# Optimization experiments

Measured on AMD Instinct MI355X. Metric: run time of the kernel, lower is better.

The kernel has to match this reference:

```python
import jax, jax.numpy as jnp
import numpy as np

B, NF, D = 8192, 64, 128


def setup_inputs() -> dict:
    key = jax.random.key(0)
    k1, k2, k3, k4 = jax.random.split(key, 4)
    F = jax.random.normal(k1, (B, NF, D), dtype=jnp.float32)
    # interaction weight tensor (num_fields, num_fields, embedding_dim)
    W = jax.random.normal(k2, (NF, NF, D), dtype=jnp.float32) * 0.05
    # torch Linear weights (out_features, in_features); y = x @ W.T
    K_w = jax.random.normal(k3, (D, D), dtype=jnp.float32) * (1.0 / np.sqrt(D))
    Q_w = jax.random.normal(k4, (D, D), dtype=jnp.float32) * (1.0 / np.sqrt(D))
    return {"F": F, "W": W, "K_w": K_w, "Q_w": Q_w}


def reference(F, W, K_w, Q_w):
    # K(F): torch Linear without bias -> F @ K_w.T, shape [B, NF, D]
    Kf = jnp.einsum('bjd,ed->bje', F, K_w)
    # S = bmm(F, K(F)^T) -> [B, NF, NF]
    S = jnp.einsum('bid,bjd->bij', F, Kf)
    # (S.unsqueeze(-1) * W).sum(dim=2) without materializing [B,NF,NF,D]
    out = jnp.einsum('bij,ijd->bid', S, W)
    # residual: Q(F)
    out = out + jnp.einsum('bid,ed->bie', F, Q_w)
    return out
```

## Files before the change

kernel.cpp:

```cpp
#include <hip/hip_runtime.h>
#include <stdint.h>

typedef _Float16 f16x8 __attribute__((ext_vector_type(8)));
typedef _Float16 f16x4 __attribute__((ext_vector_type(4)));
typedef float    f32x4 __attribute__((ext_vector_type(4)));

#define NFIELD 64
#define DIM    128
#define BTOT   8192

__global__ void prep_kernel(const float* __restrict__ W,
                            const float* __restrict__ Kw,
                            const float* __restrict__ Qw,
                            _Float16* __restrict__ Wt,
                            _Float16* __restrict__ Kh,
                            _Float16* __restrict__ Qh) {
  const int blk = blockIdx.x, t = threadIdx.x;
  if (blk < NFIELD) {
    const float* Wi = W + (size_t)blk * NFIELD * DIM;
    _Float16* Wo = Wt + (size_t)blk * DIM * NFIELD;
    for (int idx = t; idx < DIM * NFIELD; idx += 256) {
      int d = idx >> 6, j = idx & 63;
      Wo[idx] = (_Float16)Wi[j * DIM + d];
    }
  } else if (blk == NFIELD) {
    for (int idx = t; idx < DIM * DIM; idx += 256) Kh[idx] = (_Float16)Kw[idx];
  } else {
    for (int idx = t; idx < DIM * DIM; idx += 256) Qh[idx] = (_Float16)Qw[idx];
  }
}

__global__ __launch_bounds__(256, 3)
void s_kernel(const float* __restrict__ F,
              const _Float16* __restrict__ Kh,
              _Float16* __restrict__ Sg, int c0) {
  __shared__ _Float16 sF[64 * 136];
  __shared__ float    sKf[64 * 132];
  const int t = threadIdx.x;
  const int lane = t & 63, wave = t >> 6;
  const int l15 = lane & 15, quad = lane >> 4;
  const int b = c0 + blockIdx.x;
  const float* Fb = F + (size_t)b * (NFIELD * DIM);

  for (int idx = t; idx < 2048; idx += 256) {
    float4 v = ((const float4*)Fb)[idx];
    int row = idx >> 5, c4 = idx & 31;
    f16x4 h;
    h[0] = (_Float16)v.x; h[1] = (_Float16)v.y; h[2] = (_Float16)v.z; h[3] = (_Float16)v.w;
    *(f16x4*)&sF[row * 136 + c4 * 4] = h;
  }
  __syncthreads();

  f16x8 afK[4];
#pragma unroll
  for (int kt = 0; kt < 4; ++kt)
    afK[kt] = *(const f16x8*)&sF[(wave * 16 + l15) * 136 + kt * 32 + quad * 8];
#pragma unroll
  for (int et = 0; et < 8; ++et) {
    const _Float16* kp = Kh + (et * 16 + l15) * DIM + quad * 8;
    f32x4 acc = {0.f, 0.f, 0.f, 0.f};
#pragma unroll
    for (int kt = 0; kt < 4; ++kt) {
      f16x8 bf = *(const f16x8*)(kp + kt * 32);
      acc = __builtin_amdgcn_mfma_f32_16x16x32_f16(afK[kt], bf, acc, 0, 0, 0);
    }
    float* op = &sKf[(wave * 16 + quad * 4) * 132 + et * 16 + l15];
    op[0] = acc[0]; op[132] = acc[1]; op[264] = acc[2]; op[396] = acc[3];
  }
  __syncthreads();

  f32x4 accS[4];
#pragma unroll
  for (int it = 0; it < 4; ++it) accS[it] = (f32x4){0.f, 0.f, 0.f, 0.f};
#pragma unroll
  for (int kt = 0; kt < 4; ++kt) {
    const float* bp = &sKf[(wave * 16 + l15) * 132 + kt * 32 + quad * 8];
    float4 b0 = *(const float4*)bp;
    float4 b1 = *(const float4*)(bp + 4);
    f16x8 bf;
    bf[0] = (_Float16)b0.x; bf[1] = (_Float16)b0.y; bf[2] = (_Float16)b0.z; bf[3] = (_Float16)b0.w;
    bf[4] = (_Float16)b1.x; bf[5] = (_Float16)b1.y; bf[6] = (_Float16)b1.z; bf[7] = (_Float16)b1.w;
#pragma unroll
    for (int it = 0; it < 4; ++it) {
      f16x8 af = *(const f16x8*)&sF[(it * 16 + l15) * 136 + kt * 32 + quad * 8];
      accS[it] = __builtin_amdgcn_mfma_f32_16x16x32_f16(af, bf, accS[it], 0, 0, 0);
    }
  }
  _Float16* Sb = Sg + (size_t)blockIdx.x * (NFIELD * NFIELD);
#pragma unroll
  for (int it = 0; it < 4; ++it)
#pragma unroll
    for (int r = 0; r < 4; ++r)
      Sb[(it * 16 + quad * 4 + r) * 64 + wave * 16 + l15] = (_Float16)accS[it][r];
}

__global__ __launch_bounds__(256, 3)
void out_kernel(const float* __restrict__ F,
                const _Float16* __restrict__ Sg,
                const _Float16* __restrict__ Wt,
                const _Float16* __restrict__ Qh,
                float* __restrict__ Out, int c0) {
  __shared__ _Float16 sBt[128 * 200];
  const int i = blockIdx.y;
  const int t = threadIdx.x;
  const int lane = t & 63, wave = t >> 6;
  const int l15 = lane & 15, quad = lane >> 4;

  const f16x8* wp = (const f16x8*)(Wt + (size_t)i * DIM * NFIELD);
  for (int idx = t; idx < 1024; idx += 256) {
    int d = idx >> 3, jw = idx & 7;
    *(f16x8*)&sBt[d * 200 + jw * 8] = wp[idx];
  }
  const f16x8* qp = (const f16x8*)Qh;
  for (int idx = t; idx < 2048; idx += 256) {
    int d = idx >> 4, ew = idx & 15;
    *(f16x8*)&sBt[d * 200 + 64 + ew * 8] = qp[idx];
  }
  __syncthreads();

  f32x4 acc[2][8];
#pragma unroll
  for (int mi = 0; mi < 2; ++mi)
#pragma unroll
    for (int nt = 0; nt < 8; ++nt) acc[mi][nt] = (f32x4){0.f, 0.f, 0.f, 0.f};

  const int bl0 = blockIdx.x * 128;
#pragma unroll
  for (int kt = 0; kt < 6; ++kt) {
    f16x8 af[2];
#pragma unroll
    for (int mi = 0; mi < 2; ++mi) {
      const int bl = bl0 + (wave * 2 + mi) * 16 + l15;
      if (kt < 2) {
        const int j0 = kt * 32 + quad * 8;
        af[mi] = *(const f16x8*)(Sg + (size_t)bl * 4096 + i * 64 + j0);
      } else {
        const int e0 = (kt - 2) * 32 + quad * 8;
        const float* fp = F + ((size_t)(c0 + bl) * NFIELD + i) * DIM + e0;
        float4 f0 = *(const float4*)fp;
        float4 f1 = *(const float4*)(fp + 4);
        f16x8 a;
        a[0] = (_Float16)f0.x; a[1] = (_Float16)f0.y; a[2] = (_Float16)f0.z; a[3] = (_Float16)f0.w;
        a[4] = (_Float16)f1.x; a[5] = (_Float16)f1.y; a[6] = (_Float16)f1.z; a[7] = (_Float16)f1.w;
        af[mi] = a;
      }
    }
#pragma unroll
    for (int nt = 0; nt < 8; ++nt) {
      f16x8 bf = *(const f16x8*)&sBt[(nt * 16 + l15) * 200 + kt * 32 + quad * 8];
      acc[0][nt] = __builtin_amdgcn_mfma_f32_16x16x32_f16(af[0], bf, acc[0][nt], 0, 0, 0);
      acc[1][nt] = __builtin_amdgcn_mfma_f32_16x16x32_f16(af[1], bf, acc[1][nt], 0, 0, 0);
    }
  }

#pragma unroll
  for (int mi = 0; mi < 2; ++mi) {
    const int blr = bl0 + (wave * 2 + mi) * 16 + quad * 4;
#pragma unroll
    for (int nt = 0; nt < 8; ++nt) {
      const int d = nt * 16 + l15;
#pragma unroll
      for (int r = 0; r < 4; ++r) {
        const size_t gb = (size_t)(c0 + blr + r);
        Out[(gb * NFIELD + i) * DIM + d] = acc[mi][nt][r];
      }
    }
  }
}

extern "C" void kernel_launch(void* const* d_in, const int* in_sizes, int n_in,
                              void* d_out, int out_size, void* d_ws, size_t ws_size,
                              hipStream_t stream) {
  const float* F  = (const float*)d_in[0];
  const float* W  = (const float*)d_in[1];
  const float* Kw = (const float*)d_in[2];
  const float* Qw = (const float*)d_in[3];
  float* Out = (float*)d_out;

  _Float16* Wt = (_Float16*)d_ws;
  _Float16* Kh = Wt + (size_t)NFIELD * DIM * NFIELD;
  _Float16* Qh = Kh + DIM * DIM;
  _Float16* Sg = Qh + DIM * DIM;
  const size_t fixed_bytes = ((size_t)NFIELD * DIM * NFIELD + 2 * DIM * DIM) * sizeof(_Float16);
  size_t avail = (ws_size > fixed_bytes) ? (ws_size - fixed_bytes) : 0;
  int CB = BTOT;
  while (CB > 128 && (size_t)CB * NFIELD * NFIELD * sizeof(_Float16) > avail) CB >>= 1;

  prep_kernel<<<dim3(NFIELD + 2), 256, 0, stream>>>(W, Kw, Qw, Wt, Kh, Qh);
  for (int c0 = 0; c0 < BTOT; c0 += CB) {
    s_kernel<<<dim3(CB), 256, 0, stream>>>(F, Kh, Sg, c0);
    out_kernel<<<dim3(CB / 128, NFIELD), 256, 0, stream>>>(F, Sg, Wt, Qh, Out, c0);
  }
}
```

Before: 650.4 us.

## Persist S kernel over 8 batches with double-buffered F prefetch and swizzled LDS

The S kernel now handles 8 batch elements per block. It keeps the K weights in registers, double-buffers F in LDS with register prefetch of the next batch, and stores intermediates as fp16 in XOR-swizzled LDS to avoid bank conflicts. S output is staged in LDS and written with coalesced 16-byte stores one iteration later. The out kernel issues all S and F global loads before the barrier so they overlap the weight staging. Launch bounds drop to 2 blocks per CU, which raises the register budget but lowers occupancy. Kf is now rounded to fp16, which may change accuracy slightly.

Measured after the change: 606.4 us. 1.07x faster.

```diff
diff --git a/kernel.cpp b/kernel.cpp
--- a/kernel.cpp
+++ b/kernel.cpp
@@ -8,6 +8,14 @@
 #define NFIELD 64
 #define DIM    128
 #define BTOT   8192
+#define NB     8
+
+__device__ __forceinline__ f16x8 cvt8(float4 a, float4 b) {
+  f16x8 h;
+  h[0] = (_Float16)a.x; h[1] = (_Float16)a.y; h[2] = (_Float16)a.z; h[3] = (_Float16)a.w;
+  h[4] = (_Float16)b.x; h[5] = (_Float16)b.y; h[6] = (_Float16)b.z; h[7] = (_Float16)b.w;
+  return h;
+}
 
 __global__ void prep_kernel(const float* __restrict__ W,
                             const float* __restrict__ Kw,
@@ -30,92 +38,206 @@
   }
 }
 
-__global__ __launch_bounds__(256, 3)
+__global__ __launch_bounds__(256, 2)
 void s_kernel(const float* __restrict__ F,
               const _Float16* __restrict__ Kh,
               _Float16* __restrict__ Sg, int c0) {
-  __shared__ _Float16 sF[64 * 136];
-  __shared__ float    sKf[64 * 132];
+  __shared__ __attribute__((aligned(16))) _Float16 sF[2][64 * 128];
+  __shared__ __attribute__((aligned(16))) _Float16 sKf[64 * 128];
+  __shared__ __attribute__((aligned(16))) _Float16 sS[2][64 * 64];
   const int t = threadIdx.x;
   const int lane = t & 63, wave = t >> 6;
   const int l15 = lane & 15, quad = lane >> 4;
-  const int b = c0 + blockIdx.x;
-  const float* Fb = F + (size_t)b * (NFIELD * DIM);
-
-  for (int idx = t; idx < 2048; idx += 256) {
-    float4 v = ((const float4*)Fb)[idx];
-    int row = idx >> 5, c4 = idx & 31;
-    f16x4 h;
-    h[0] = (_Float16)v.x; h[1] = (_Float16)v.y; h[2] = (_Float16)v.z; h[3] = (_Float16)v.w;
-    *(f16x4*)&sF[row * 136 + c4 * 4] = h;
+  const int bbase = blockIdx.x * NB;
+
+  f16x8 kh[2][4];
+#pragma unroll
+  for (int eh = 0; eh < 2; ++eh)
+#pragma unroll
+    for (int kt = 0; kt < 4; ++kt)
+      kh[eh][kt] = *(const f16x8*)(Kh + ((wave * 2 + eh) * 16 + l15) * DIM + kt * 32 + quad * 8);
+
+  float4 fr[8];
+  {
+    const float4* Fb4 = (const float4*)(F + (size_t)(c0 + bbase) * (NFIELD * DIM));
+#pragma unroll
+    for (int k = 0; k < 4; ++k) {
+      int u = t + k * 256;
+      fr[2 * k]     = Fb4[2 * u];
+      fr[2 * k + 1] = Fb4[2 * u + 1];
+    }
+#pragma unroll
+    for (int k = 0; k < 4; ++k) {
+      int u = t + k * 256;
+      int row = u >> 4, c8 = u & 15;
+      *(f16x8*)((char*)&sF[0][0] + row * 256 + ((c8 * 16) ^ ((row & 7) << 4))) =
+          cvt8(fr[2 * k], fr[2 * k + 1]);
+    }
+  }
+  {
+    const float4* Fb4 = (const float4*)(F + (size_t)(c0 + bbase + 1) * (NFIELD * DIM));
+#pragma unroll
+    for (int k = 0; k < 4; ++k) {
+      int u = t + k * 256;
+      fr[2 * k]     = Fb4[2 * u];
+      fr[2 * k + 1] = Fb4[2 * u + 1];
+    }
   }
   __syncthreads();
 
-  f16x8 afK[4];
-#pragma unroll
-  for (int kt = 0; kt < 4; ++kt)
-    afK[kt] = *(const f16x8*)&sF[(wave * 16 + l15) * 136 + kt * 32 + quad * 8];
-#pragma unroll
-  for (int et = 0; et < 8; ++et) {
-    const _Float16* kp = Kh + (et * 16 + l15) * DIM + quad * 8;
-    f32x4 acc = {0.f, 0.f, 0.f, 0.f};
+  for (int bi = 0; bi < NB; ++bi) {
+    const int cur = bi & 1;
+    const _Float16* sFc = &sF[cur][0];
+
+    f16x8 afc[4][4];
+#pragma unroll
+    for (int jt = 0; jt < 4; ++jt)
+#pragma unroll
+      for (int kt = 0; kt < 4; ++kt) {
+        int row = jt * 16 + l15;
+        afc[jt][kt] = *(const f16x8*)((const char*)sFc + row * 256 +
+                                      ((kt * 64 + quad * 16) ^ ((row & 7) << 4)));
+      }
+    f32x4 aKf[4][2];
+#pragma unroll
+    for (int jt = 0; jt < 4; ++jt) {
+      aKf[jt][0] = (f32x4){0.f, 0.f, 0.f, 0.f};
+      aKf[jt][1] = (f32x4){0.f, 0.f, 0.f, 0.f};
+    }
+#pragma unroll
+    for (int jt = 0; jt < 4; ++jt)
+#pragma unroll
+      for (int kt = 0; kt < 4; ++kt) {
+        aKf[jt][0] = __builtin_amdgcn_mfma_f32_16x16x32_f16(afc[jt][kt], kh[0][kt], aKf[jt][0], 0, 0, 0);
+        aKf[jt][1] = __builtin_amdgcn_mfma_f32_16x16x32_f16(afc[jt][kt], kh[1][kt], aKf[jt][1], 0, 0, 0);
+      }
+#pragma unroll
+    for (int jt = 0; jt < 4; ++jt)
+#pragma unroll
+      for (int eh = 0; eh < 2; ++eh) {
+        int e = (wave * 2 + eh) * 16 + l15;
+#pragma unroll
+        for (int r = 0; r < 4; ++r) {
+          int j = jt * 16 + quad * 4 + r;
+          *(_Float16*)((char*)sKf + j * 256 + ((e * 2) ^ ((j & 7) << 4))) =
+              (_Float16)aKf[jt][eh][r];
+        }
+      }
+    if (bi + 1 < NB) {
+#pragma unroll
+      for (int k = 0; k < 4; ++k) {
+        int u = t + k * 256;
+        int row = u >> 4, c8 = u & 15;
+        *(f16x8*)((char*)&sF[cur ^ 1][0] + row * 256 + ((c8 * 16) ^ ((row & 7) << 4))) =
+            cvt8(fr[2 * k], fr[2 * k + 1]);
+      }
+    }
+    __syncthreads();
+
+    if (bi + 2 < NB) {
+      const float4* Fb4 = (const float4*)(F + (size_t)(c0 + bbase + bi + 2) * (NFIELD * DIM));
+#pragma unroll
+      for (int k = 0; k < 4; ++k) {
+        int u = t + k * 256;
+        fr[2 * k]     = Fb4[2 * u];
+        fr[2 * k + 1] = Fb4[2 * u + 1];
+      }
+    }
+
+    if (bi > 0) {
+      _Float16* dst = Sg + (size_t)(bbase + bi - 1) * (NFIELD * NFIELD);
+#pragma unroll
+      for (int k = 0; k < 2; ++k) {
+        int idx = t + k * 256;
+        int si = idx >> 3, j8 = idx & 7;
+        f16x8 v = *(const f16x8*)((const char*)&sS[cur ^ 1][0] + si * 128 +
+                                  ((j8 * 16) ^ ((si & 7) << 4)));
+        *(f16x8*)(dst + si * 64 + j8 * 8) = v;
+      }
+    }
+
+    f16x8 bS[4];
 #pragma unroll
     for (int kt = 0; kt < 4; ++kt) {
-      f16x8 bf = *(const f16x8*)(kp + kt * 32);
-      acc = __builtin_amdgcn_mfma_f32_16x16x32_f16(afK[kt], bf, acc, 0, 0, 0);
-    }
-    float* op = &sKf[(wave * 16 + quad * 4) * 132 + et * 16 + l15];
-    op[0] = acc[0]; op[132] = acc[1]; op[264] = acc[2]; op[396] = acc[3];
-  }
-  __syncthreads();
-
-  f32x4 accS[4];
-#pragma unroll
-  for (int it = 0; it < 4; ++it) accS[it] = (f32x4){0.f, 0.f, 0.f, 0.f};
-#pragma unroll
-  for (int kt = 0; kt < 4; ++kt) {
-    const float* bp = &sKf[(wave * 16 + l15) * 132 + kt * 32 + quad * 8];
-    float4 b0 = *(const float4*)bp;
-    float4 b1 = *(const float4*)(bp + 4);
-    f16x8 bf;
-    bf[0] = (_Float16)b0.x; bf[1] = (_Float16)b0.y; bf[2] = (_Float16)b0.z; bf[3] = (_Float16)b0.w;
-    bf[4] = (_Float16)b1.x; bf[5] = (_Float16)b1.y; bf[6] = (_Float16)b1.z; bf[7] = (_Float16)b1.w;
-#pragma unroll
-    for (int it = 0; it < 4; ++it) {
-      f16x8 af = *(const f16x8*)&sF[(it * 16 + l15) * 136 + kt * 32 + quad * 8];
-      accS[it] = __builtin_amdgcn_mfma_f32_16x16x32_f16(af, bf, accS[it], 0, 0, 0);
-    }
-  }
-  _Float16* Sb = Sg + (size_t)blockIdx.x * (NFIELD * NFIELD);
-#pragma unroll
-  for (int it = 0; it < 4; ++it)
-#pragma unroll
-    for (int r = 0; r < 4; ++r)
-      Sb[(it * 16 + quad * 4 + r) * 64 + wave * 16 + l15] = (_Float16)accS[it][r];
-}
-
-__global__ __launch_bounds__(256, 3)
+      int row = wave * 16 + l15;
+      bS[kt] = *(const f16x8*)((const char*)sKf + row * 256 +
+                               ((kt * 64 + quad * 16) ^ ((row & 7) << 4)));
+    }
+    f32x4 aS[4];
+#pragma unroll
+    for (int it = 0; it < 4; ++it) aS[it] = (f32x4){0.f, 0.f, 0.f, 0.f};
+#pragma unroll
+    for (int it = 0; it < 4; ++it)
+#pragma unroll
+      for (int kt = 0; kt < 4; ++kt)
+        aS[it] = __builtin_amdgcn_mfma_f32_16x16x32_f16(afc[it][kt], bS[kt], aS[it], 0, 0, 0);
+#pragma unroll
+    for (int it = 0; it < 4; ++it)
+#pragma unroll
+      for (int r = 0; r < 4; ++r) {
+        int si = it * 16 + quad * 4 + r, j = wave * 16 + l15;
+        *(_Float16*)((char*)&sS[cur][0] + si * 128 + ((j * 2) ^ ((si & 7) << 4))) =
+            (_Float16)aS[it][r];
+      }
+    __syncthreads();
+  }
+  {
+    const int cur = (NB - 1) & 1;
+    _Float16* dst = Sg + (size_t)(bbase + NB - 1) * (NFIELD * NFIELD);
+#pragma unroll
+    for (int k = 0; k < 2; ++k) {
+      int idx = t + k * 256;
+      int si = idx >> 3, j8 = idx & 7;
+      f16x8 v = *(const f16x8*)((const char*)&sS[cur][0] + si * 128 +
+                                ((j8 * 16) ^ ((si & 7) << 4)));
+      *(f16x8*)(dst + si * 64 + j8 * 8) = v;
+    }
+  }
+}
+
+__global__ __launch_bounds__(256, 2)
 void out_kernel(const float* __restrict__ F,
                 const _Float16* __restrict__ Sg,
                 const _Float16* __restrict__ Wt,
                 const _Float16* __restrict__ Qh,
                 float* __restrict__ Out, int c0) {
-  __shared__ _Float16 sBt[128 * 200];
+  __shared__ __attribute__((aligned(16))) _Float16 sBt[128 * 200];
   const int i = blockIdx.y;
   const int t = threadIdx.x;
   const int lane = t & 63, wave = t >> 6;
   const int l15 = lane & 15, quad = lane >> 4;
 
   const f16x8* wp = (const f16x8*)(Wt + (size_t)i * DIM * NFIELD);
-  for (int idx = t; idx < 1024; idx += 256) {
+#pragma unroll
+  for (int k = 0; k < 4; ++k) {
+    int idx = t + k * 256;
     int d = idx >> 3, jw = idx & 7;
     *(f16x8*)&sBt[d * 200 + jw * 8] = wp[idx];
   }
   const f16x8* qp = (const f16x8*)Qh;
-  for (int idx = t; idx < 2048; idx += 256) {
+#pragma unroll
+  for (int k = 0; k < 8; ++k) {
+    int idx = t + k * 256;
     int d = idx >> 4, ew = idx & 15;
     *(f16x8*)&sBt[d * 200 + 64 + ew * 8] = qp[idx];
   }
+
+  const int bl0 = blockIdx.x * 128;
+  f16x8 aS[2][2];
+  float4 fr[2][8];
+#pragma unroll
+  for (int mi = 0; mi < 2; ++mi) {
+    const int bl = bl0 + (wave * 2 + mi) * 16 + l15;
+#pragma unroll
+    for (int kt = 0; kt < 2; ++kt)
+      aS[mi][kt] = *(const f16x8*)(Sg + (size_t)bl * 4096 + i * 64 + kt * 32 + quad * 8);
+    const float* fp = F + ((size_t)(c0 + bl) * NFIELD + i) * DIM + quad * 8;
+#pragma unroll
+    for (int kt = 0; kt < 4; ++kt) {
+      fr[mi][2 * kt]     = *(const float4*)(fp + kt * 32);
+      fr[mi][2 * kt + 1] = *(const float4*)(fp + kt * 32 + 4);
+    }
+  }
   __syncthreads();
 
   f32x4 acc[2][8];
@@ -124,26 +246,13 @@
 #pragma unroll
     for (int nt = 0; nt < 8; ++nt) acc[mi][nt] = (f32x4){0.f, 0.f, 0.f, 0.f};
 
-  const int bl0 = blockIdx.x * 128;
 #pragma unroll
   for (int kt = 0; kt < 6; ++kt) {
     f16x8 af[2];
 #pragma unroll
     for (int mi = 0; mi < 2; ++mi) {
-      const int bl = bl0 + (wave * 2 + mi) * 16 + l15;
-      if (kt < 2) {
-        const int j0 = kt * 32 + quad * 8;
-        af[mi] = *(const f16x8*)(Sg + (size_t)bl * 4096 + i * 64 + j0);
-      } else {
-        const int e0 = (kt - 2) * 32 + quad * 8;
-        const float* fp = F + ((size_t)(c0 + bl) * NFIELD + i) * DIM + e0;
-        float4 f0 = *(const float4*)fp;
-        float4 f1 = *(const float4*)(fp + 4);
-        f16x8 a;
-        a[0] = (_Float16)f0.x; a[1] = (_Float16)f0.y; a[2] = (_Float16)f0.z; a[3] = (_Float16)f0.w;
-        a[4] = (_Float16)f1.x; a[5] = (_Float16)f1.y; a[6] = (_Float16)f1.z; a[7] = (_Float16)f1.w;
-        af[mi] = a;
-      }
+      if (kt < 2) af[mi] = aS[mi][kt];
+      else        af[mi] = cvt8(fr[mi][2 * (kt - 2)], fr[mi][2 * (kt - 2) + 1]);
     }
 #pragma unroll
     for (int nt = 0; nt < 8; ++nt) {
@@ -188,7 +297,7 @@
 
   prep_kernel<<<dim3(NFIELD + 2), 256, 0, stream>>>(W, Kw, Qw, Wt, Kh, Qh);
   for (int c0 = 0; c0 < BTOT; c0 += CB) {
-    s_kernel<<<dim3(CB), 256, 0, stream>>>(F, Kh, Sg, c0);
+    s_kernel<<<dim3(CB / NB), 256, 0, stream>>>(F, Kh, Sg, c0);
     out_kernel<<<dim3(CB / 128, NFIELD), 256, 0, stream>>>(F, Sg, Wt, Qh, Out, c0);
   }
 }
```
